# Performance work log

Measured on AMD Instinct MI355X. Metric: run time of the kernel, lower is better.

Reference implementation:

```python
import jax, jax.numpy as jnp
import numpy as np

NUM_CODES = 4096
CODE_DIM = 256
COMMITMENT_COST = 0.25
DIVERSITY_WEIGHT = 0.1
B = 65536


def setup_inputs() -> dict:
    key = jax.random.key(0)
    kz, ke = jax.random.split(key)
    z = jax.random.normal(kz, (B, CODE_DIM), dtype=jnp.float32)
    embedding = jax.random.normal(ke, (NUM_CODES, CODE_DIM), dtype=jnp.float32)
    return {"z": z, "embedding": embedding}


def reference(z, embedding):
    # distances [B, K] = ||z||^2 + ||e||^2 - 2 z e^T
    distances = (
        jnp.sum(z * z, axis=1, keepdims=True)
        + jnp.sum(embedding * embedding, axis=1)
        - 2.0 * z @ embedding.T
    )
    indices = jnp.argmin(distances, axis=1)  # [B] int
    z_q = embedding[indices]                  # [B, D]

    sg = jax.lax.stop_gradient
    commitment_loss = jnp.mean((z - sg(z_q)) ** 2)
    embedding_loss = jnp.mean((sg(z) - z_q) ** 2)

    # diversity regularizer over soft assignments
    soft = jax.nn.softmax(-distances, axis=1)        # [B, K]
    avg_soft = jnp.mean(soft, axis=0)                # [K]
    entropy = -jnp.sum(avg_soft * jnp.log(avg_soft + 1e-10))
    max_entropy = jnp.log(jnp.float32(NUM_CODES))
    diversity_loss = max_entropy - entropy

    vq_loss = (
        commitment_loss * COMMITMENT_COST
        + embedding_loss
        + DIVERSITY_WEIGHT * diversity_loss
    )

    # straight-through estimator
    z_q_st = z + sg(z_q - z)

    # perplexity from hard assignments (bincount == one-hot mean)
    avg_probs = jnp.bincount(indices, length=NUM_CODES).astype(jnp.float32) / B
    perplexity = jnp.exp(-jnp.sum(avg_probs * jnp.log(avg_probs + 1e-10)))

    return (z_q_st, vq_loss, perplexity, indices, diversity_loss)
```

## Files before the change

kernel.cpp:

```cpp
#include <hip/hip_runtime.h>
#include <cstdint>
#include <cstddef>


#define NROWS     65536
#define NCODES    4096
#define DDIM      256
#define CAND_CAP  24
#define MARGIN    0.5f
#define NPART     64

typedef _Float16 half8 __attribute__((ext_vector_type(8)));
typedef _Float16 half4 __attribute__((ext_vector_type(4)));
typedef float    f32x4 __attribute__((ext_vector_type(4)));

#define WS_CANDCNT  0u
#define WS_BINCNT   262144u
#define WS_SPARTG   278528u
#define WS_ZERO_END 1327104u
#define WS_EF16     1327104u
#define WS_ZZ       3424256u
#define WS_EE       3686400u
#define WS_ROWD     3702784u
#define WS_CANDIDX  3964928u
#define WS_TE       10256384u
#define WS_TP       10289152u
#define WS_END      10321920u

__device__ __forceinline__ void gload_lds16(const void* g, void* lds) {
    __builtin_amdgcn_global_load_lds(
        (const __attribute__((address_space(1))) unsigned int*)g,
        (__attribute__((address_space(3))) unsigned int*)lds, 16, 0, 0);
}

__global__ __launch_bounds__(256)
void prep_kernel(const float* __restrict__ src, _Float16* __restrict__ dst,
                 float* __restrict__ norms)
{
    const int tid = threadIdx.x;
    const int w = tid >> 6, l = tid & 63;
    const int row = blockIdx.x * 4 + w;
    const float4 v = *(const float4*)(src + (size_t)row * DDIM + l * 4);
    half4 h;
    h[0] = (_Float16)v.x; h[1] = (_Float16)v.y;
    h[2] = (_Float16)v.z; h[3] = (_Float16)v.w;
    *(half4*)(dst + (size_t)row * DDIM + l * 4) = h;
    double s = (double)v.x * v.x + (double)v.y * v.y
             + (double)v.z * v.z + (double)v.w * v.w;
#pragma unroll
    for (int off = 1; off < 64; off <<= 1) s += __shfl_xor(s, off, 64);
    if (l == 0) norms[row] = (float)s;
}

__global__ __launch_bounds__(256, 2)
void sweep_fused_kernel(const _Float16* __restrict__ zf, const _Float16* __restrict__ ef,
                        const float* __restrict__ zz, const float* __restrict__ ee,
                        float* __restrict__ SpartG, int* __restrict__ cand_cnt,
                        int* __restrict__ cand_idx)
{
    __shared__ _Float16 Bl[128 * 256];
    __shared__ float eel[128];

    const int tid = threadIdx.x;
    const int w = tid >> 6, l = tid & 63;
    const int lg = l >> 4, lc = l & 15;
    const int row0 = blockIdx.x * 128;

    half8 af[2][8];
#pragma unroll
    for (int fr = 0; fr < 2; ++fr)
#pragma unroll
        for (int ksl = 0; ksl < 8; ++ksl)
            af[fr][ksl] = *(const half8*)(zf + (size_t)(row0 + w * 32 + fr * 16 + lc) * DDIM
                                          + ksl * 32 + lg * 8);

    float zr[8];
#pragma unroll
    for (int fr = 0; fr < 2; ++fr)
#pragma unroll
        for (int reg = 0; reg < 4; ++reg)
            zr[fr * 4 + reg] = zz[row0 + w * 32 + fr * 16 + lg * 4 + reg];

    const char* efb = (const char*)ef;
    char* blb = (char*)Bl;

    float pm[8], pZ[8];
#pragma unroll
    for (int i = 0; i < 8; ++i) { pm[i] = 1e30f; pZ[i] = 0.0f; }

    for (int phase = 0; phase < 2; ++phase) {
        for (int nt = 0; nt < 32; ++nt) {
            __syncthreads();
#pragma unroll
            for (int it = 0; it < 16; ++it) {
                const int p = it * 4096 + w * 1024 + l * 16;
                const int brow = p >> 9;
                const int cby = (p & 511) ^ ((brow & 7) << 4);
                gload_lds16(efb + (((size_t)(nt * 128 + brow)) << 9) + cby,
                            blb + it * 4096 + w * 1024);
            }
            if (tid < 128) eel[tid] = ee[nt * 128 + tid];
            __syncthreads();

            f32x4 acc[2][8];
#pragma unroll
            for (int fr = 0; fr < 2; ++fr)
#pragma unroll
                for (int cf = 0; cf < 8; ++cf) acc[fr][cf] = (f32x4){0.f, 0.f, 0.f, 0.f};

            const char* bbase = blb + ((size_t)lc << 9);
#pragma unroll
            for (int ksl = 0; ksl < 8; ++ksl) {
                const char* bp = bbase + (((ksl * 64 + lg * 16) ^ ((lc & 7) << 4)));
#pragma unroll
                for (int cf = 0; cf < 8; ++cf) {
                    const half8 b = *(const half8*)(bp + cf * 8192);
                    acc[0][cf] = __builtin_amdgcn_mfma_f32_16x16x32_f16(af[0][ksl], b, acc[0][cf], 0, 0, 0);
                    acc[1][cf] = __builtin_amdgcn_mfma_f32_16x16x32_f16(af[1][ksl], b, acc[1][cf], 0, 0, 0);
                }
            }

            float eev[8];
#pragma unroll
            for (int cf = 0; cf < 8; ++cf) eev[cf] = eel[cf * 16 + lc];

            if (phase == 0) {
#pragma unroll
                for (int fr = 0; fr < 2; ++fr)
#pragma unroll
                for (int reg = 0; reg < 4; ++reg) {
                    const int ri = fr * 4 + reg;
                    const float zrv = zr[ri];
                    float m = pm[ri], Zv = pZ[ri];
#pragma unroll
                    for (int cf = 0; cf < 8; ++cf) {
                        const float d = fmaf(-2.0f, acc[fr][cf][reg], zrv + eev[cf]);
                        const float mn = fminf(m, d);
                        Zv = fmaf(Zv, __expf(mn - m), __expf(mn - d));
                        m = mn;
                    }
                    pm[ri] = m; pZ[ri] = Zv;
                }
            } else {
                float sp[8];
#pragma unroll
                for (int cf = 0; cf < 8; ++cf) sp[cf] = 0.0f;
#pragma unroll
                for (int fr = 0; fr < 2; ++fr)
#pragma unroll
                for (int reg = 0; reg < 4; ++reg) {
                    const int ri = fr * 4 + reg;
                    const float zrv = zr[ri];
                    const float m = pm[ri], iz = pZ[ri];
#pragma unroll
                    for (int cf = 0; cf < 8; ++cf) {
                        const float d = fmaf(-2.0f, acc[fr][cf][reg], zrv + eev[cf]);
                        sp[cf] += __expf(m - d) * iz;
                        if (d <= m + MARGIN) {
                            const int rg_ = row0 + w * 32 + fr * 16 + lg * 4 + reg;
                            const int slot = atomicAdd(&cand_cnt[rg_], 1);
                            if (slot < CAND_CAP)
                                cand_idx[(size_t)rg_ * CAND_CAP + slot] = nt * 128 + cf * 16 + lc;
                        }
                    }
                }
#pragma unroll
                for (int cf = 0; cf < 8; ++cf) {
                    float v = sp[cf];
                    v += __shfl_xor(v, 16, 64);
                    v += __shfl_xor(v, 32, 64);
                    if (l < 16)
                        atomicAdd(&SpartG[(size_t)(blockIdx.x & (NPART - 1)) * NCODES
                                          + nt * 128 + cf * 16 + l], v);
                }
            }
        }

        if (phase == 0) {
#pragma unroll
            for (int ri = 0; ri < 8; ++ri) {
                float m = pm[ri], Zv = pZ[ri];
#pragma unroll
                for (int off = 1; off < 16; off <<= 1) {
                    const float mo = __shfl_xor(m, off, 64);
                    const float Zo = __shfl_xor(Zv, off, 64);
                    const float mn = fminf(m, mo);
                    Zv = fmaf(Zv, __expf(mn - m), Zo * __expf(mn - mo));
                    m = mn;
                }
                pm[ri] = m;
                pZ[ri] = 1.0f / Zv;
            }
        }
    }
}

__global__ __launch_bounds__(256)
void refine_kernel(const float* __restrict__ z, const float* __restrict__ emb,
                   const int* __restrict__ cand_cnt, const int* __restrict__ cand_idx,
                   float* __restrict__ out_zq, float* __restrict__ out_idx,
                   unsigned int* __restrict__ bincnt, float* __restrict__ rowD)
{
    const int tid = threadIdx.x;
    const int w = tid >> 6, l = tid & 63;
    const int row = blockIdx.x * 4 + w;
    const float4 zv = *(const float4*)(z + (size_t)row * DDIM + l * 4);
    const double z0 = zv.x, z1 = zv.y, z2 = zv.z, z3 = zv.w;
    const int craw = cand_cnt[row];
    const int cnt = craw < 1 ? 1 : (craw > CAND_CAP ? CAND_CAP : craw);
    double dmin = 1e300; int kmin = 0;
    for (int c = 0; c < cnt; ++c) {
        int k = (craw < 1) ? 0 : cand_idx[(size_t)row * CAND_CAP + c];
        k &= (NCODES - 1);
        const float4 ev = *(const float4*)(emb + (size_t)k * DDIM + l * 4);
        const double t0 = z0 - ev.x, t1 = z1 - ev.y, t2 = z2 - ev.z, t3 = z3 - ev.w;
        double s = t0 * t0 + t1 * t1 + t2 * t2 + t3 * t3;
#pragma unroll
        for (int off = 1; off < 64; off <<= 1) s += __shfl_xor(s, off, 64);
        if (s < dmin || (s == dmin && k < kmin)) { dmin = s; kmin = k; }
    }
    const float4 bv = *(const float4*)(emb + (size_t)kmin * DDIM + l * 4);
    *(float4*)(out_zq + (size_t)row * DDIM + l * 4) = bv;
    if (l == 0) {
        out_idx[row] = (float)kmin;
        atomicAdd(&bincnt[kmin], 1u);
        rowD[row] = (float)dmin;
    }
}

__global__ __launch_bounds__(256)
void reduce1_kernel(const float* __restrict__ Spart, const unsigned int* __restrict__ bincnt,
                    const float* __restrict__ rowD,
                    double* __restrict__ te, double* __restrict__ tp, double* __restrict__ tm)
{
    const int k = blockIdx.x * 256 + threadIdx.x;
    double s = 0.0;
#pragma unroll 8
    for (int p = 0; p < NPART; ++p) s += (double)Spart[(size_t)p * NCODES + k];
    const double avg = s * (1.0 / 65536.0);
    te[k] = avg * log(avg + 1e-10);
    const double ap = (double)bincnt[k] * (1.0 / 65536.0);
    tp[k] = ap * log(ap + 1e-10);
    double dm = 0.0;
#pragma unroll
    for (int j = 0; j < 16; ++j) dm += (double)rowD[k * 16 + j];
    tm[k] = dm;
}

__global__ __launch_bounds__(256)
void reduce2_kernel(const double* __restrict__ te, const double* __restrict__ tp,
                    const double* __restrict__ tm, float* __restrict__ out)
{
    __shared__ double sa[256], sb[256], sc[256];
    const int tid = threadIdx.x;
    double a = 0.0, b = 0.0, c = 0.0;
    for (int i = tid; i < NCODES; i += 256) { a += te[i]; b += tp[i]; c += tm[i]; }
    sa[tid] = a; sb[tid] = b; sc[tid] = c;
    __syncthreads();
    for (int s = 128; s > 0; s >>= 1) {
        if (tid < s) { sa[tid] += sa[tid + s]; sb[tid] += sb[tid + s]; sc[tid] += sc[tid + s]; }
        __syncthreads();
    }
    if (tid == 0) {
        const double entropy    = -sa[0];
        const double diversity  = log(4096.0) - entropy;
        const double perplexity = exp(-sb[0]);
        const double mse        = sc[0] * (1.0 / 16777216.0);
        const double vq         = 1.25 * mse + 0.1 * diversity;
        out[16777216] = (float)vq;
        out[16777217] = (float)perplexity;
        out[16842754] = (float)diversity;
    }
}

extern "C" void kernel_launch(void* const* d_in, const int* in_sizes, int n_in,
                              void* d_out, int out_size, void* d_ws, size_t ws_size,
                              hipStream_t stream)
{
    const float* z   = (const float*)d_in[0];
    const float* emb = (const float*)d_in[1];
    float* out = (float*)d_out;
    char* ws = (char*)d_ws;
    if (ws_size < (size_t)WS_END) return;

    int*          cand_cnt = (int*)(ws + WS_CANDCNT);
    unsigned int* bincnt   = (unsigned int*)(ws + WS_BINCNT);
    float*        SpartG   = (float*)(ws + WS_SPARTG);
    _Float16*     ef16     = (_Float16*)(ws + WS_EF16);
    float*        zz       = (float*)(ws + WS_ZZ);
    float*        ee       = (float*)(ws + WS_EE);
    float*        rowD     = (float*)(ws + WS_ROWD);
    int*          cand_idx = (int*)(ws + WS_CANDIDX);
    double*       te       = (double*)(ws + WS_TE);
    double*       tp       = (double*)(ws + WS_TP);
    double*       tm       = (double*)(ws + WS_CANDIDX);

    _Float16* zf16 = (_Float16*)d_out;

    hipMemsetAsync(d_ws, 0, WS_ZERO_END, stream);
    hipLaunchKernelGGL(prep_kernel, dim3(NROWS / 4), dim3(256), 0, stream, z, zf16, zz);
    hipLaunchKernelGGL(prep_kernel, dim3(NCODES / 4), dim3(256), 0, stream, emb, ef16, ee);
    hipLaunchKernelGGL(sweep_fused_kernel, dim3(NROWS / 128), dim3(256), 0, stream,
                       zf16, ef16, zz, ee, SpartG, cand_cnt, cand_idx);
    hipLaunchKernelGGL(refine_kernel, dim3(NROWS / 4), dim3(256), 0, stream,
                       z, emb, cand_cnt, cand_idx, out, out + 16777218, bincnt, rowD);
    hipLaunchKernelGGL(reduce1_kernel, dim3(16), dim3(256), 0, stream, SpartG, bincnt, rowD, te, tp, tm);
    hipLaunchKernelGGL(reduce2_kernel, dim3(1), dim3(256), 0, stream, te, tp, tm, out);
}
```

Baseline: 525.7 us.

## Double-buffer codebook tiles, drop z prep pass, accumulate soft sums in LDS

The sweep kernel now converts z to fp16 in registers directly, which removes the separate z prep launch and its zz norms. The row norm is dropped from the distance because it cancels inside the softmax and the argmin margin. Codebook tiles shrink to 64 codes and are double-buffered, so the next tile's global-to-LDS load overlaps the current MFMA work with a single barrier per step. Per-code soft-assignment sums go into an LDS array and are written as one partial per block. That replaces the global atomics into 64 partitions, but reduce1 must now read 512 partials per code. The online softmax update is restructured to rescale once per group of four codes.

```diff
diff --git a/kernel.cpp b/kernel.cpp
--- a/kernel.cpp
+++ b/kernel.cpp
@@ -8,7 +8,6 @@
 #define DDIM      256
 #define CAND_CAP  24
 #define MARGIN    0.5f
-#define NPART     64
 
 typedef _Float16 half8 __attribute__((ext_vector_type(8)));
 typedef _Float16 half4 __attribute__((ext_vector_type(4)));
@@ -16,16 +15,15 @@
 
 #define WS_CANDCNT  0u
 #define WS_BINCNT   262144u
-#define WS_SPARTG   278528u
-#define WS_ZERO_END 1327104u
-#define WS_EF16     1327104u
-#define WS_ZZ       3424256u
-#define WS_EE       3686400u
-#define WS_ROWD     3702784u
-#define WS_CANDIDX  3964928u
-#define WS_TE       10256384u
-#define WS_TP       10289152u
-#define WS_END      10321920u
+#define WS_ZERO_END 278528u
+#define WS_SPART    278528u
+#define WS_EF16     8667136u
+#define WS_EE       10764288u
+#define WS_ROWD     10780672u
+#define WS_CANDIDX  11042816u
+#define WS_TE       17334272u
+#define WS_TP       17367040u
+#define WS_END      17399808u
 
 __device__ __forceinline__ void gload_lds16(const void* g, void* lds) {
     __builtin_amdgcn_global_load_lds(
@@ -53,13 +51,12 @@
 }
 
 __global__ __launch_bounds__(256, 2)
-void sweep_fused_kernel(const _Float16* __restrict__ zf, const _Float16* __restrict__ ef,
-                        const float* __restrict__ zz, const float* __restrict__ ee,
-                        float* __restrict__ SpartG, int* __restrict__ cand_cnt,
-                        int* __restrict__ cand_idx)
-{
-    __shared__ _Float16 Bl[128 * 256];
-    __shared__ float eel[128];
+void sweep_fused_kernel(const float* __restrict__ z, const _Float16* __restrict__ ef,
+                        const float* __restrict__ ee, float* __restrict__ Spart,
+                        int* __restrict__ cand_cnt, int* __restrict__ cand_idx)
+{
+    __shared__ _Float16 Bl[2][64 * 256];
+    __shared__ float Sl[NCODES];
 
     const int tid = threadIdx.x;
     const int w = tid >> 6, l = tid & 63;
@@ -70,113 +67,120 @@
 #pragma unroll
     for (int fr = 0; fr < 2; ++fr)
 #pragma unroll
-        for (int ksl = 0; ksl < 8; ++ksl)
-            af[fr][ksl] = *(const half8*)(zf + (size_t)(row0 + w * 32 + fr * 16 + lc) * DDIM
-                                          + ksl * 32 + lg * 8);
-
-    float zr[8];
-#pragma unroll
-    for (int fr = 0; fr < 2; ++fr)
-#pragma unroll
-        for (int reg = 0; reg < 4; ++reg)
-            zr[fr * 4 + reg] = zz[row0 + w * 32 + fr * 16 + lg * 4 + reg];
-
+    for (int ksl = 0; ksl < 8; ++ksl) {
+        const float* zp = z + (size_t)(row0 + w * 32 + fr * 16 + lc) * DDIM + ksl * 32 + lg * 8;
+        const float4 v0 = *(const float4*)zp;
+        const float4 v1 = *(const float4*)(zp + 4);
+        half8 h;
+        h[0] = (_Float16)v0.x; h[1] = (_Float16)v0.y; h[2] = (_Float16)v0.z; h[3] = (_Float16)v0.w;
+        h[4] = (_Float16)v1.x; h[5] = (_Float16)v1.y; h[6] = (_Float16)v1.z; h[7] = (_Float16)v1.w;
+        af[fr][ksl] = h;
+    }
+
+    for (int i = tid; i < NCODES; i += 256) Sl[i] = 0.0f;
+
+    int soff[8];
+#pragma unroll
+    for (int it = 0; it < 8; ++it) {
+        const int p = w * 8192 + it * 1024 + l * 16;
+        const int brow = p >> 9;
+        soff[it] = (brow << 9) + ((p & 511) ^ ((brow & 7) << 4));
+    }
     const char* efb = (const char*)ef;
-    char* blb = (char*)Bl;
+    char* blb = (char*)&Bl[0][0];
 
     float pm[8], pZ[8];
 #pragma unroll
     for (int i = 0; i < 8; ++i) { pm[i] = 1e30f; pZ[i] = 0.0f; }
 
-    for (int phase = 0; phase < 2; ++phase) {
-        for (int nt = 0; nt < 32; ++nt) {
-            __syncthreads();
-#pragma unroll
-            for (int it = 0; it < 16; ++it) {
-                const int p = it * 4096 + w * 1024 + l * 16;
-                const int brow = p >> 9;
-                const int cby = (p & 511) ^ ((brow & 7) << 4);
-                gload_lds16(efb + (((size_t)(nt * 128 + brow)) << 9) + cby,
-                            blb + it * 4096 + w * 1024);
-            }
-            if (tid < 128) eel[tid] = ee[nt * 128 + tid];
-            __syncthreads();
-
-            f32x4 acc[2][8];
+#pragma unroll
+    for (int it = 0; it < 8; ++it)
+        gload_lds16(efb + soff[it], blb + w * 8192 + it * 1024);
+    __syncthreads();
+
+    const int xorv = (lc & 7) << 4;
+    const char* bRd0 = blb + (lc << 9);
+
+    for (int s = 0; s < 128; ++s) {
+        const int cur = s & 1;
+        const int nt = s & 63;
+
+        if (s < 127) {
+            const int nnt = (s + 1) & 63;
+            const char* src = efb + ((size_t)nnt << 15);
+            char* dst = blb + (cur ^ 1) * 32768 + w * 8192;
+#pragma unroll
+            for (int it = 0; it < 8; ++it)
+                gload_lds16(src + soff[it], dst + it * 1024);
+        }
+
+        float eev[4];
+#pragma unroll
+        for (int cf = 0; cf < 4; ++cf) eev[cf] = ee[nt * 64 + cf * 16 + lc];
+
+        f32x4 acc[2][4];
+#pragma unroll
+        for (int fr = 0; fr < 2; ++fr)
+#pragma unroll
+            for (int cf = 0; cf < 4; ++cf) acc[fr][cf] = (f32x4){0.f, 0.f, 0.f, 0.f};
+
+        const char* bb = bRd0 + cur * 32768;
+#pragma unroll
+        for (int ksl = 0; ksl < 8; ++ksl) {
+            const int ko = (ksl * 64 + lg * 16) ^ xorv;
+#pragma unroll
+            for (int cf = 0; cf < 4; ++cf) {
+                const half8 b = *(const half8*)(bb + cf * 8192 + ko);
+                acc[0][cf] = __builtin_amdgcn_mfma_f32_16x16x32_f16(af[0][ksl], b, acc[0][cf], 0, 0, 0);
+                acc[1][cf] = __builtin_amdgcn_mfma_f32_16x16x32_f16(af[1][ksl], b, acc[1][cf], 0, 0, 0);
+            }
+        }
+
+        if (s < 64) {
 #pragma unroll
             for (int fr = 0; fr < 2; ++fr)
 #pragma unroll
-                for (int cf = 0; cf < 8; ++cf) acc[fr][cf] = (f32x4){0.f, 0.f, 0.f, 0.f};
-
-            const char* bbase = blb + ((size_t)lc << 9);
-#pragma unroll
-            for (int ksl = 0; ksl < 8; ++ksl) {
-                const char* bp = bbase + (((ksl * 64 + lg * 16) ^ ((lc & 7) << 4)));
-#pragma unroll
-                for (int cf = 0; cf < 8; ++cf) {
-                    const half8 b = *(const half8*)(bp + cf * 8192);
-                    acc[0][cf] = __builtin_amdgcn_mfma_f32_16x16x32_f16(af[0][ksl], b, acc[0][cf], 0, 0, 0);
-                    acc[1][cf] = __builtin_amdgcn_mfma_f32_16x16x32_f16(af[1][ksl], b, acc[1][cf], 0, 0, 0);
-                }
-            }
-
-            float eev[8];
-#pragma unroll
-            for (int cf = 0; cf < 8; ++cf) eev[cf] = eel[cf * 16 + lc];
-
-            if (phase == 0) {
-#pragma unroll
-                for (int fr = 0; fr < 2; ++fr)
-#pragma unroll
-                for (int reg = 0; reg < 4; ++reg) {
-                    const int ri = fr * 4 + reg;
-                    const float zrv = zr[ri];
-                    float m = pm[ri], Zv = pZ[ri];
-#pragma unroll
-                    for (int cf = 0; cf < 8; ++cf) {
-                        const float d = fmaf(-2.0f, acc[fr][cf][reg], zrv + eev[cf]);
-                        const float mn = fminf(m, d);
-                        Zv = fmaf(Zv, __expf(mn - m), __expf(mn - d));
-                        m = mn;
-                    }
-                    pm[ri] = m; pZ[ri] = Zv;
-                }
-            } else {
-                float sp[8];
-#pragma unroll
-                for (int cf = 0; cf < 8; ++cf) sp[cf] = 0.0f;
-#pragma unroll
-                for (int fr = 0; fr < 2; ++fr)
-#pragma unroll
-                for (int reg = 0; reg < 4; ++reg) {
-                    const int ri = fr * 4 + reg;
-                    const float zrv = zr[ri];
-                    const float m = pm[ri], iz = pZ[ri];
-#pragma unroll
-                    for (int cf = 0; cf < 8; ++cf) {
-                        const float d = fmaf(-2.0f, acc[fr][cf][reg], zrv + eev[cf]);
-                        sp[cf] += __expf(m - d) * iz;
-                        if (d <= m + MARGIN) {
-                            const int rg_ = row0 + w * 32 + fr * 16 + lg * 4 + reg;
-                            const int slot = atomicAdd(&cand_cnt[rg_], 1);
-                            if (slot < CAND_CAP)
-                                cand_idx[(size_t)rg_ * CAND_CAP + slot] = nt * 128 + cf * 16 + lc;
-                        }
+            for (int reg = 0; reg < 4; ++reg) {
+                const int ri = fr * 4 + reg;
+                const float d0 = fmaf(-2.0f, acc[fr][0][reg], eev[0]);
+                const float d1 = fmaf(-2.0f, acc[fr][1][reg], eev[1]);
+                const float d2 = fmaf(-2.0f, acc[fr][2][reg], eev[2]);
+                const float d3 = fmaf(-2.0f, acc[fr][3][reg], eev[3]);
+                const float mloc = fminf(fminf(d0, d1), fminf(d2, d3));
+                float m = pm[ri];
+                if (mloc < m) { pZ[ri] *= __expf(mloc - m); m = mloc; pm[ri] = m; }
+                pZ[ri] += __expf(m - d0) + __expf(m - d1) + __expf(m - d2) + __expf(m - d3);
+            }
+        } else {
+            float sp[4] = {0.f, 0.f, 0.f, 0.f};
+#pragma unroll
+            for (int fr = 0; fr < 2; ++fr)
+#pragma unroll
+            for (int reg = 0; reg < 4; ++reg) {
+                const int ri = fr * 4 + reg;
+                const float m = pm[ri], iz = pZ[ri];
+#pragma unroll
+                for (int cf = 0; cf < 4; ++cf) {
+                    const float d = fmaf(-2.0f, acc[fr][cf][reg], eev[cf]);
+                    sp[cf] += __expf(m - d) * iz;
+                    if (d <= m + MARGIN) {
+                        const int rg_ = row0 + w * 32 + fr * 16 + lg * 4 + reg;
+                        const int slot = atomicAdd(&cand_cnt[rg_], 1);
+                        if (slot < CAND_CAP)
+                            cand_idx[(size_t)rg_ * CAND_CAP + slot] = nt * 64 + cf * 16 + lc;
                     }
                 }
-#pragma unroll
-                for (int cf = 0; cf < 8; ++cf) {
-                    float v = sp[cf];
-                    v += __shfl_xor(v, 16, 64);
-                    v += __shfl_xor(v, 32, 64);
-                    if (l < 16)
-                        atomicAdd(&SpartG[(size_t)(blockIdx.x & (NPART - 1)) * NCODES
-                                          + nt * 128 + cf * 16 + l], v);
-                }
+            }
+#pragma unroll
+            for (int cf = 0; cf < 4; ++cf) {
+                float v = sp[cf];
+                v += __shfl_xor(v, 16, 64);
+                v += __shfl_xor(v, 32, 64);
+                if (l < 16) atomicAdd(&Sl[nt * 64 + cf * 16 + l], v);
             }
         }
 
-        if (phase == 0) {
+        if (s == 63) {
 #pragma unroll
             for (int ri = 0; ri < 8; ++ri) {
                 float m = pm[ri], Zv = pZ[ri];
@@ -185,14 +189,19 @@
                     const float mo = __shfl_xor(m, off, 64);
                     const float Zo = __shfl_xor(Zv, off, 64);
                     const float mn = fminf(m, mo);
-                    Zv = fmaf(Zv, __expf(mn - m), Zo * __expf(mn - mo));
+                    Zv = Zv * __expf(mn - m) + Zo * __expf(mn - mo);
                     m = mn;
                 }
                 pm[ri] = m;
                 pZ[ri] = 1.0f / Zv;
             }
         }
-    }
+
+        __syncthreads();
+    }
+
+    for (int i = tid; i < NCODES; i += 256)
+        Spart[(size_t)blockIdx.x * NCODES + i] = Sl[i];
 }
 
 __global__ __launch_bounds__(256)
@@ -236,7 +245,7 @@
     const int k = blockIdx.x * 256 + threadIdx.x;
     double s = 0.0;
 #pragma unroll 8
-    for (int p = 0; p < NPART; ++p) s += (double)Spart[(size_t)p * NCODES + k];
+    for (int wg = 0; wg < 512; ++wg) s += (double)Spart[(size_t)wg * NCODES + k];
     const double avg = s * (1.0 / 65536.0);
     te[k] = avg * log(avg + 1e-10);
     const double ap = (double)bincnt[k] * (1.0 / 65536.0);
@@ -285,9 +294,8 @@
 
     int*          cand_cnt = (int*)(ws + WS_CANDCNT);
     unsigned int* bincnt   = (unsigned int*)(ws + WS_BINCNT);
-    float*        SpartG   = (float*)(ws + WS_SPARTG);
+    float*        Spart    = (float*)(ws + WS_SPART);
     _Float16*     ef16     = (_Float16*)(ws + WS_EF16);
-    float*        zz       = (float*)(ws + WS_ZZ);
     float*        ee       = (float*)(ws + WS_EE);
     float*        rowD     = (float*)(ws + WS_ROWD);
     int*          cand_idx = (int*)(ws + WS_CANDIDX);
@@ -295,15 +303,12 @@
     double*       tp       = (double*)(ws + WS_TP);
     double*       tm       = (double*)(ws + WS_CANDIDX);
 
-    _Float16* zf16 = (_Float16*)d_out;
-
     hipMemsetAsync(d_ws, 0, WS_ZERO_END, stream);
-    hipLaunchKernelGGL(prep_kernel, dim3(NROWS / 4), dim3(256), 0, stream, z, zf16, zz);
     hipLaunchKernelGGL(prep_kernel, dim3(NCODES / 4), dim3(256), 0, stream, emb, ef16, ee);
     hipLaunchKernelGGL(sweep_fused_kernel, dim3(NROWS / 128), dim3(256), 0, stream,
-                       zf16, ef16, zz, ee, SpartG, cand_cnt, cand_idx);
+                       z, ef16, ee, Spart, cand_cnt, cand_idx);
     hipLaunchKernelGGL(refine_kernel, dim3(NROWS / 4), dim3(256), 0, stream,
                        z, emb, cand_cnt, cand_idx, out, out + 16777218, bincnt, rowD);
-    hipLaunchKernelGGL(reduce1_kernel, dim3(16), dim3(256), 0, stream, SpartG, bincnt, rowD, te, tp, tm);
+    hipLaunchKernelGGL(reduce1_kernel, dim3(16), dim3(256), 0, stream, Spart, bincnt, rowD, te, tp, tm);
     hipLaunchKernelGGL(reduce2_kernel, dim3(1), dim3(256), 0, stream, te, tp, tm, out);
 }
```

New measurement: 459.0 us. -12.7%, faster.
